# Optimization experiments

Measured on AMD Instinct MI355X. Metric: run time of the kernel, lower is better.

## Reference

```python
import jax, jax.numpy as jnp
import numpy as np

DQ = 256  # query feature size
DK = 256  # key feature size
DV = 256  # value feature size
B, SQ, SK = 4, 256, 256
D = DQ + DK  # MLP hidden width (512)


def setup_inputs() -> dict:
    key = jax.random.key(0)
    ks = jax.random.split(key, 7)
    Q = jax.random.normal(ks[0], (B, SQ, DQ), dtype=jnp.float32)
    K = jax.random.normal(ks[1], (B, SK, DK), dtype=jnp.float32)
    V = jax.random.normal(ks[2], (B, SK, DV), dtype=jnp.float32)
    # key-padding style mask: True = masked out. Keep at least the first key
    # unmasked so softmax rows are well-behaved.
    mask_out = jax.random.randint(ks[3], (B, 1, SK), 0, 2).astype(jnp.bool_)
    mask_out = mask_out.at[:, :, 0].set(False)
    # nn.Linear(D, D, bias=True): weight [D, D], bias [D]
    lim1 = 1.0 / np.sqrt(D)
    W1 = jax.random.uniform(ks[4], (D, D), minval=-lim1, maxval=lim1, dtype=jnp.float32)
    b1 = jax.random.uniform(ks[5], (D,), minval=-lim1, maxval=lim1, dtype=jnp.float32)
    # nn.Linear(D, 1, bias=False): weight [1, D] -> store as vector [D]
    W2 = jax.random.uniform(ks[6], (D,), minval=-lim1, maxval=lim1, dtype=jnp.float32)
    return {"Q": Q, "K": K, "V": V, "mask_out": mask_out, "W1": W1, "b1": b1, "W2": W2}


def reference(Q, K, V, mask_out, W1, b1, W2):
    # Concat-then-Linear splits: cat([q,k]) @ W1.T == q @ W1[:, :DQ].T + k @ W1[:, DQ:].T
    q_h = jnp.einsum('bqd,hd->bqh', Q, W1[:, :DQ])          # [B,SQ,D]
    k_h = jnp.einsum('bkd,hd->bkh', K, W1[:, DQ:])          # [B,SK,D]
    hidden = q_h[:, :, None, :] + k_h[:, None, :, :] + b1   # [B,SQ,SK,D]
    act = jax.nn.leaky_relu(hidden, negative_slope=0.01)
    scores = jnp.einsum('bqkh,h->bqk', act, W2)             # [B,SQ,SK]
    scores = jnp.where(mask_out, jnp.float32(-1e9), scores)
    attn = jax.nn.softmax(scores, axis=-1)
    return jnp.einsum('bqk,bkv->bqv', attn, V)              # [B,SQ,DV]
```

## Files before the change

kernel.cpp:

```cpp
#include <hip/hip_runtime.h>

#define HH_OFF 0
#define KT_OFF (1024 * 512)

typedef short short8 __attribute__((ext_vector_type(8)));
typedef float f32x4 __attribute__((ext_vector_type(4)));

union S8 {
  short8 v;
  unsigned short s[8];
};

__device__ __forceinline__ unsigned bf16rne(float x) {
  unsigned u = __float_as_uint(x);
  u += 0x7FFFu + ((u >> 16) & 1u);
  return u >> 16;
}

__device__ __forceinline__ void cvt_split8(const float4& f0, const float4& f1,
                                           short8& hv8, short8& lv8) {
  float xs[8] = {f0.x, f0.y, f0.z, f0.w, f1.x, f1.y, f1.z, f1.w};
  S8 hv, lv;
#pragma unroll
  for (int e = 0; e < 8; ++e) {
    unsigned u = __float_as_uint(xs[e]);
    unsigned hu = u & 0xFFFF0000u;
    hv.s[e] = (unsigned short)(hu >> 16);
    float lo = xs[e] - __uint_as_float(hu);
    unsigned ul = __float_as_uint(lo);
    ul += 0x7FFFu + ((ul >> 16) & 1u);
    lv.s[e] = (unsigned short)(ul >> 16);
  }
  hv8 = hv.v;
  lv8 = lv.v;
}

__global__ __launch_bounds__(512) void gemm_k(const float* __restrict__ Q,
                                              const float* __restrict__ Kin,
                                              const float* __restrict__ W1,
                                              const float* __restrict__ b1,
                                              float* __restrict__ hh,
                                              unsigned* __restrict__ kT2) {
  __shared__ short AH[64 * 32], AL[64 * 32], BH[64 * 32], BL[64 * 32];
  const int t = threadIdx.x;
  const int blk = blockIdx.x;
  const bool isK = blk >= 128;
  const float *A, *B;
  int lda, ldb, m0, n0, aoff;
  if (!isK) {
    int bm = blk >> 3, bn = blk & 7;
    m0 = bm * 64; n0 = bn * 64;
    A = Q;   lda = 256; aoff = 0;
    B = W1;  ldb = 512;
  } else {
    int t2 = blk - 128;
    int bm = t2 >> 4, bn = t2 & 15;
    m0 = bm * 64; n0 = bn * 64;
    A = W1;  lda = 512; aoff = 256;
    B = Kin; ldb = 256;
  }
  const int mat = t >> 8;
  const int cc = t & 255;
  const int sr = cc >> 2;
  const int c8 = (cc & 3) * 8;
  const float* srcbase =
      mat ? (B + (size_t)(n0 + sr) * ldb + c8)
          : (A + (size_t)(m0 + sr) * lda + aoff + c8);
  short* dstH = (mat ? BH : AH) + sr * 32 + c8;
  short* dstL = (mat ? BL : AL) + sr * 32 + c8;

  const int w = t >> 6, lane = t & 63;
  const int wr = (w >> 2) * 32, wc = (w & 3) * 16;
  const int lane15 = lane & 15, lk8 = (lane >> 4) * 8;

  f32x4 acc[2] = {{0.f, 0.f, 0.f, 0.f}, {0.f, 0.f, 0.f, 0.f}};

  float4 f0 = *(const float4*)&srcbase[0];
  float4 f1 = *(const float4*)&srcbase[4];
  for (int ks = 0; ks < 8; ++ks) {
    short8 hv8, lv8;
    cvt_split8(f0, f1, hv8, lv8);
    __syncthreads();
    *(short8*)dstH = hv8;
    *(short8*)dstL = lv8;
    __syncthreads();
    if (ks < 7) {
      f0 = *(const float4*)&srcbase[(ks + 1) * 32];
      f1 = *(const float4*)&srcbase[(ks + 1) * 32 + 4];
    }
    short8 ah0 = *(const short8*)&AH[(wr + lane15) * 32 + lk8];
    short8 ah1 = *(const short8*)&AH[(wr + 16 + lane15) * 32 + lk8];
    short8 al0 = *(const short8*)&AL[(wr + lane15) * 32 + lk8];
    short8 al1 = *(const short8*)&AL[(wr + 16 + lane15) * 32 + lk8];
    short8 bh = *(const short8*)&BH[(wc + lane15) * 32 + lk8];
    short8 bl = *(const short8*)&BL[(wc + lane15) * 32 + lk8];
    acc[0] = __builtin_amdgcn_mfma_f32_16x16x32_bf16(ah0, bh, acc[0], 0, 0, 0);
    acc[1] = __builtin_amdgcn_mfma_f32_16x16x32_bf16(ah1, bh, acc[1], 0, 0, 0);
    acc[0] = __builtin_amdgcn_mfma_f32_16x16x32_bf16(ah0, bl, acc[0], 0, 0, 0);
    acc[1] = __builtin_amdgcn_mfma_f32_16x16x32_bf16(ah1, bl, acc[1], 0, 0, 0);
    acc[0] = __builtin_amdgcn_mfma_f32_16x16x32_bf16(al0, bh, acc[0], 0, 0, 0);
    acc[1] = __builtin_amdgcn_mfma_f32_16x16x32_bf16(al1, bh, acc[1], 0, 0, 0);
  }
  const int lg4 = (lane >> 4) * 4;
  if (!isK) {
#pragma unroll
    for (int i = 0; i < 2; ++i) {
#pragma unroll
      for (int reg = 0; reg < 4; ++reg) {
        int row = m0 + wr + i * 16 + lg4 + reg;
        hh[(size_t)row * 512 + n0 + wc + lane15] = acc[i][reg];
      }
    }
  } else {
    const int col = n0 + wc + lane15;
#pragma unroll
    for (int i = 0; i < 2; ++i) {
      int r0 = m0 + wr + i * 16 + lg4;
      float v0 = acc[i][0] + b1[r0 + 0];
      float v1 = acc[i][1] + b1[r0 + 1];
      float v2 = acc[i][2] + b1[r0 + 2];
      float v3 = acc[i][3] + b1[r0 + 3];
      unsigned p01 = bf16rne(v0) | (bf16rne(v1) << 16);
      unsigned p23 = bf16rne(v2) | (bf16rne(v3) << 16);
      int hp = r0 >> 1;
      kT2[(size_t)hp * 1024 + col] = p01;
      kT2[(size_t)(hp + 1) * 1024 + col] = p23;
    }
  }
}

__global__ __launch_bounds__(512) void attn_k(const float* __restrict__ hh,
                                              const unsigned* __restrict__ kT2,
                                              const float* __restrict__ V,
                                              const void* __restrict__ maskp,
                                              const float* __restrict__ W2,
                                              float* __restrict__ out) {
  __shared__ float smem[14016];
  __shared__ int sflag;
  float* att = smem;
  float* rowsum = smem + 1040;
  float* qlin = smem + 1044;
  float* qs = smem + 1056;
  float* w2s = smem + 3104;
  float* sabs = smem + 3616;
  float* klin = smem + 11936;
  float* red = smem + 3616;

  const int t = threadIdx.x;
  const int blk = blockIdx.x;
  const int b = blk >> 6;
  const int q4 = blk & 63;
  const int w = t >> 6, lane = t & 63;

  if (t == 0) sflag = 0;
  {
    const float* qbase = hh + (size_t)(b * 256 + q4 * 4) * 512;
    int row = t >> 7, c4 = (t & 127) * 4;
    *(float4*)&qs[row * 512 + c4] = *(const float4*)&qbase[(size_t)row * 512 + c4];
    if (t < 128) *(float4*)&w2s[t * 4] = *(const float4*)&W2[t * 4];
  }
  __syncthreads();
  if (t < 256) {
    const unsigned char* mb = (const unsigned char*)maskp;
    int nz = mb[t * 4 + 1] | mb[t * 4 + 2] | mb[t * 4 + 3];
    if (nz) atomicOr(&sflag, 1);
  }
  if (w < 4) {
    float p = 0.f;
#pragma unroll
    for (int u = 0; u < 8; ++u)
      p = fmaf(w2s[lane + 64 * u], qs[w * 512 + lane + 64 * u], p);
#pragma unroll
    for (int o = 32; o; o >>= 1) p += __shfl_xor(p, o, 64);
    if (lane == 0) qlin[w] = 0.505f * p;
  }
  {
    float sa[4][4] = {};
    float kl[4] = {};
    const unsigned* kTb = kT2 + (size_t)b * 256 + lane * 4;
    const int hbase = w * 64;
    const int hp0 = hbase >> 1;
    uint4 ua = *(const uint4*)&kTb[(size_t)hp0 * 1024];
    uint4 ub = *(const uint4*)&kTb[(size_t)(hp0 + 1) * 1024];
#pragma unroll
    for (int hg = 0; hg < 16; ++hg) {
      const int h = hbase + hg * 4;
      uint4 na, nb;
      if (hg < 15) {
        na = *(const uint4*)&kTb[(size_t)((h + 4) >> 1) * 1024];
        nb = *(const uint4*)&kTb[(size_t)(((h + 4) >> 1) + 1) * 1024];
      }
      float w24[4], qv[4][4];
      *(float4*)w24 = *(const float4*)&w2s[h];
#pragma unroll
      for (int q = 0; q < 4; ++q)
        *(float4*)qv[q] = *(const float4*)&qs[q * 512 + h];
      unsigned uac[4] = {ua.x, ua.y, ua.z, ua.w};
      unsigned ubc[4] = {ub.x, ub.y, ub.z, ub.w};
      float kv[4][4];
#pragma unroll
      for (int c = 0; c < 4; ++c) {
        kv[0][c] = __uint_as_float(uac[c] << 16);
        kv[1][c] = __uint_as_float(uac[c] & 0xFFFF0000u);
        kv[2][c] = __uint_as_float(ubc[c] << 16);
        kv[3][c] = __uint_as_float(ubc[c] & 0xFFFF0000u);
      }
#pragma unroll
      for (int e = 0; e < 4; ++e) {
#pragma unroll
        for (int c = 0; c < 4; ++c) {
          kl[c] = fmaf(w24[e], kv[e][c], kl[c]);
#pragma unroll
          for (int q = 0; q < 4; ++q) {
            float tt = qv[q][e] + kv[e][c];
            sa[q][c] = fmaf(w24[e], fabsf(tt), sa[q][c]);
          }
        }
      }
      ua = na;
      ub = nb;
    }
    const int k0 = lane * 4;
#pragma unroll
    for (int q = 0; q < 4; ++q)
      *(float4*)&sabs[(w * 4 + q) * 260 + k0] =
          make_float4(sa[q][0], sa[q][1], sa[q][2], sa[q][3]);
    *(float4*)&klin[w * 260 + k0] = make_float4(kl[0], kl[1], kl[2], kl[3]);
  }
  __syncthreads();
  if (t < 256) {
    const int flag = sflag;
    const unsigned char* m8 = (const unsigned char*)maskp;
    const int* m32 = (const int*)maskp;
    bool masked = flag ? (m8[b * 256 + t] != 0) : (m32[b * 256 + t] != 0);
    float kls = 0.f;
#pragma unroll
    for (int ww = 0; ww < 8; ++ww) kls += klin[ww * 260 + t];
    kls *= 0.505f;
#pragma unroll
    for (int q = 0; q < 4; ++q) {
      float v = 0.f;
#pragma unroll
      for (int ww = 0; ww < 8; ++ww) v += sabs[(ww * 4 + q) * 260 + t];
      v = qlin[q] + kls + 0.495f * v;
      att[q * 260 + t] = masked ? -1e9f : v;
    }
  }
  __syncthreads();
  if (w < 4) {
    float m = -1e30f;
#pragma unroll
    for (int u = 0; u < 4; ++u) m = fmaxf(m, att[w * 260 + lane + 64 * u]);
#pragma unroll
    for (int o = 32; o; o >>= 1) m = fmaxf(m, __shfl_xor(m, o, 64));
    float ssum = 0.f;
#pragma unroll
    for (int u = 0; u < 4; ++u) {
      float e = __expf(att[w * 260 + lane + 64 * u] - m);
      att[w * 260 + lane + 64 * u] = e;
      ssum += e;
    }
#pragma unroll
    for (int o = 32; o; o >>= 1) ssum += __shfl_xor(ssum, o, 64);
    if (lane == 0) rowsum[w] = ssum;
  }
  __syncthreads();
  {
    const int v0 = lane * 4;
    const float* Vb = V + (size_t)b * 65536;
    float acc[4][4] = {};
#pragma unroll 1
    for (int kk = 0; kk < 32; ++kk) {
      int k = w * 32 + kk;
      float4 vv = *(const float4*)&Vb[(size_t)k * 256 + v0];
      float aw[4];
#pragma unroll
      for (int q = 0; q < 4; ++q) aw[q] = att[q * 260 + k];
#pragma unroll
      for (int q = 0; q < 4; ++q) {
        acc[q][0] = fmaf(aw[q], vv.x, acc[q][0]);
        acc[q][1] = fmaf(aw[q], vv.y, acc[q][1]);
        acc[q][2] = fmaf(aw[q], vv.z, acc[q][2]);
        acc[q][3] = fmaf(aw[q], vv.w, acc[q][3]);
      }
    }
#pragma unroll
    for (int q = 0; q < 4; ++q)
      *(float4*)&red[(w * 4 + q) * 264 + v0] =
          make_float4(acc[q][0], acc[q][1], acc[q][2], acc[q][3]);
  }
  __syncthreads();
#pragma unroll
  for (int s = 0; s < 2; ++s) {
    int id = t + s * 512;
    int row = id >> 8, col = id & 255;
    float v = 0.f;
#pragma unroll
    for (int g = 0; g < 8; ++g) v += red[(g * 4 + row) * 264 + col];
    out[((size_t)b * 256 + q4 * 4 + row) * 256 + col] = v / rowsum[row];
  }
}

extern "C" void kernel_launch(void* const* d_in, const int* in_sizes, int n_in,
                              void* d_out, int out_size, void* d_ws,
                              size_t ws_size, hipStream_t stream) {
  const float* Q = (const float*)d_in[0];
  const float* K = (const float*)d_in[1];
  const float* V = (const float*)d_in[2];
  const void* mask = d_in[3];
  const float* W1 = (const float*)d_in[4];
  const float* b1 = (const float*)d_in[5];
  const float* W2 = (const float*)d_in[6];
  float* ws = (float*)d_ws;
  float* hh = ws + HH_OFF;
  unsigned* kT2 = (unsigned*)(ws + KT_OFF);
  float* out = (float*)d_out;

  gemm_k<<<dim3(256), dim3(512), 0, stream>>>(Q, K, W1, b1, hh, kT2);
  attn_k<<<dim3(256), dim3(512), 0, stream>>>(hh, kT2, V, mask, W2, out);
}
```

Before: 33.28 us.

## Compact unmasked keys and skip score and PV work for masked keys

Builds a compacted list of unmasked key indices per batch with a ballot and prefix count, then computes the MLP scores and the attention-times-V accumulation only over those keys. Masked keys get -1e9 written directly. Roughly half the keys are masked, so this removes that share of the score FLOPs and V loads. In exchange the kT loads become scalar gathers instead of coalesced uint4 loads, and the change adds two extra block barriers plus a data-dependent loop.

```diff
diff --git a/kernel.cpp b/kernel.cpp
--- a/kernel.cpp
+++ b/kernel.cpp
@@ -136,7 +136,9 @@
                                               const float* __restrict__ W2,
                                               float* __restrict__ out) {
   __shared__ float smem[14016];
-  __shared__ int sflag;
+  __shared__ int sflag, nkS;
+  __shared__ int wsumS[4];
+  __shared__ int kidxS[256];
   float* att = smem;
   float* rowsum = smem + 1040;
   float* qlin = smem + 1044;
@@ -174,65 +176,93 @@
     for (int o = 32; o; o >>= 1) p += __shfl_xor(p, o, 64);
     if (lane == 0) qlin[w] = 0.505f * p;
   }
-  {
-    float sa[4][4] = {};
-    float kl[4] = {};
-    const unsigned* kTb = kT2 + (size_t)b * 256 + lane * 4;
-    const int hbase = w * 64;
-    const int hp0 = hbase >> 1;
-    uint4 ua = *(const uint4*)&kTb[(size_t)hp0 * 1024];
-    uint4 ub = *(const uint4*)&kTb[(size_t)(hp0 + 1) * 1024];
-#pragma unroll
-    for (int hg = 0; hg < 16; ++hg) {
-      const int h = hbase + hg * 4;
-      uint4 na, nb;
-      if (hg < 15) {
-        na = *(const uint4*)&kTb[(size_t)((h + 4) >> 1) * 1024];
-        nb = *(const uint4*)&kTb[(size_t)(((h + 4) >> 1) + 1) * 1024];
-      }
-      float w24[4], qv[4][4];
-      *(float4*)w24 = *(const float4*)&w2s[h];
-#pragma unroll
-      for (int q = 0; q < 4; ++q)
-        *(float4*)qv[q] = *(const float4*)&qs[q * 512 + h];
-      unsigned uac[4] = {ua.x, ua.y, ua.z, ua.w};
-      unsigned ubc[4] = {ub.x, ub.y, ub.z, ub.w};
-      float kv[4][4];
-#pragma unroll
-      for (int c = 0; c < 4; ++c) {
-        kv[0][c] = __uint_as_float(uac[c] << 16);
-        kv[1][c] = __uint_as_float(uac[c] & 0xFFFF0000u);
-        kv[2][c] = __uint_as_float(ubc[c] << 16);
-        kv[3][c] = __uint_as_float(ubc[c] & 0xFFFF0000u);
-      }
-#pragma unroll
-      for (int e = 0; e < 4; ++e) {
-#pragma unroll
-        for (int c = 0; c < 4; ++c) {
-          kl[c] = fmaf(w24[e], kv[e][c], kl[c]);
-#pragma unroll
-          for (int q = 0; q < 4; ++q) {
-            float tt = qv[q][e] + kv[e][c];
-            sa[q][c] = fmaf(w24[e], fabsf(tt), sa[q][c]);
-          }
-        }
-      }
-      ua = na;
-      ub = nb;
-    }
-    const int k0 = lane * 4;
-#pragma unroll
-    for (int q = 0; q < 4; ++q)
-      *(float4*)&sabs[(w * 4 + q) * 260 + k0] =
-          make_float4(sa[q][0], sa[q][1], sa[q][2], sa[q][3]);
-    *(float4*)&klin[w * 260 + k0] = make_float4(kl[0], kl[1], kl[2], kl[3]);
-  }
-  __syncthreads();
+  __syncthreads();
+  bool act = false;
+  int pre = 0;
   if (t < 256) {
     const int flag = sflag;
     const unsigned char* m8 = (const unsigned char*)maskp;
     const int* m32 = (const int*)maskp;
-    bool masked = flag ? (m8[b * 256 + t] != 0) : (m32[b * 256 + t] != 0);
+    act = flag ? (m8[b * 256 + t] == 0) : (m32[b * 256 + t] == 0);
+    unsigned long long bal = __ballot(act);
+    pre = __popcll(bal & ((1ull << lane) - 1ull));
+    if (lane == 0) wsumS[w] = __popcll(bal);
+  }
+  __syncthreads();
+  if (t < 256 && act) {
+    int off = 0;
+#pragma unroll
+    for (int ww = 0; ww < 4; ++ww)
+      if (ww < w) off += wsumS[ww];
+    kidxS[off + pre] = t;
+  }
+  if (t == 0) nkS = wsumS[0] + wsumS[1] + wsumS[2] + wsumS[3];
+  __syncthreads();
+  const int nk = nkS;
+  const int ncg = (nk + 63) >> 6;
+
+  {
+    float sa[4][4] = {};
+    float kl[4] = {};
+    const unsigned* kTbase = kT2 + (size_t)b * 256;
+    const unsigned* colp[4];
+#pragma unroll
+    for (int cg = 0; cg < 4; ++cg) {
+      int ci = cg * 64 + lane;
+      int kc = kidxS[ci < nk ? ci : (nk - 1)];
+      colp[cg] = kTbase + kc;
+    }
+    const int hbase = w * 64;
+#pragma unroll 2
+    for (int hg = 0; hg < 16; ++hg) {
+      const int h = hbase + hg * 4;
+      const int hp = h >> 1;
+      unsigned ua[4], ub[4];
+#pragma unroll
+      for (int cg = 0; cg < 4; ++cg)
+        if (cg < ncg) {
+          ua[cg] = colp[cg][(size_t)hp * 1024];
+          ub[cg] = colp[cg][(size_t)(hp + 1) * 1024];
+        }
+      float w24[4], qv[4][4];
+      *(float4*)w24 = *(const float4*)&w2s[h];
+#pragma unroll
+      for (int q = 0; q < 4; ++q)
+        *(float4*)qv[q] = *(const float4*)&qs[q * 512 + h];
+#pragma unroll
+      for (int cg = 0; cg < 4; ++cg)
+        if (cg < ncg) {
+          float kv[4];
+          kv[0] = __uint_as_float(ua[cg] << 16);
+          kv[1] = __uint_as_float(ua[cg] & 0xFFFF0000u);
+          kv[2] = __uint_as_float(ub[cg] << 16);
+          kv[3] = __uint_as_float(ub[cg] & 0xFFFF0000u);
+#pragma unroll
+          for (int e = 0; e < 4; ++e) {
+            kl[cg] = fmaf(w24[e], kv[e], kl[cg]);
+#pragma unroll
+            for (int q = 0; q < 4; ++q)
+              sa[q][cg] = fmaf(w24[e], fabsf(qv[q][e] + kv[e]), sa[q][cg]);
+          }
+        }
+    }
+#pragma unroll
+    for (int cg = 0; cg < 4; ++cg)
+      if (cg < ncg) {
+        int ci = cg * 64 + lane;
+#pragma unroll
+        for (int q = 0; q < 4; ++q) sabs[(w * 4 + q) * 260 + ci] = sa[q][cg];
+        klin[w * 260 + ci] = kl[cg];
+      }
+  }
+  __syncthreads();
+  if (t < 256) {
+#pragma unroll
+    for (int q = 0; q < 4; ++q) att[q * 260 + t] = -1e9f;
+  }
+  __syncthreads();
+  if (t < nk) {
+    const int realk = kidxS[t];
     float kls = 0.f;
 #pragma unroll
     for (int ww = 0; ww < 8; ++ww) kls += klin[ww * 260 + t];
@@ -242,8 +272,7 @@
       float v = 0.f;
 #pragma unroll
       for (int ww = 0; ww < 8; ++ww) v += sabs[(ww * 4 + q) * 260 + t];
-      v = qlin[q] + kls + 0.495f * v;
-      att[q * 260 + t] = masked ? -1e9f : v;
+      att[q * 260 + realk] = qlin[q] + kls + 0.495f * v;
     }
   }
   __syncthreads();
@@ -269,9 +298,8 @@
     const int v0 = lane * 4;
     const float* Vb = V + (size_t)b * 65536;
     float acc[4][4] = {};
-#pragma unroll 1
-    for (int kk = 0; kk < 32; ++kk) {
-      int k = w * 32 + kk;
+    for (int i = w; i < nk; i += 8) {
+      int k = kidxS[i];
       float4 vv = *(const float4*)&Vb[(size_t)k * 256 + v0];
       float aw[4];
 #pragma unroll
```

Result: slower. 34.76 us (+4.4%).
